# Kernel tuning notes

Hardware: AMD Instinct MI355X
Metric: run time of the kernel (lower is better)

## Reference

```python
import jax, jax.numpy as jnp
import numpy as np
import math

H = 16          # num_heads
BS = 512        # block_size


def setup_inputs() -> dict:
    key = jax.random.key(0)
    ks = jax.random.split(key, 5)
    B, S, D = 2, 8192, 1024
    return {
        "x": jax.random.normal(ks[0], (B, S, D), dtype=jnp.float32),
        "W_qkv": jax.random.normal(ks[1], (D, 3 * D), dtype=jnp.float32) * (1.0 / math.sqrt(D)),
        "b_qkv": jax.random.normal(ks[2], (3 * D,), dtype=jnp.float32) * 0.02,
        "W_out": jax.random.normal(ks[3], (D, D), dtype=jnp.float32) * (1.0 / math.sqrt(D)),
        "b_out": jax.random.normal(ks[4], (D,), dtype=jnp.float32) * 0.02,
    }


def reference(x, W_qkv, b_qkv, W_out, b_out):
    B, S, D = x.shape
    hd = D // H
    nb = S // BS  # S chosen divisible by block_size, so no padding branch
    scale = 1.0 / math.sqrt(hd)

    qkv = (x @ W_qkv + b_qkv).reshape(B, S, 3, H, hd)
    qkv = jnp.transpose(qkv, (2, 0, 3, 1, 4))  # [3, B, H, S, hd]
    q, k, v = qkv[0], qkv[1], qkv[2]

    # split into blocks: [B, H, nb, BS, hd]
    qb = q.reshape(B, H, nb, BS, hd)
    kb = k.reshape(B, H, nb, BS, hd)
    vb = v.reshape(B, H, nb, BS, hd)

    # local block attention (separate softmax, as in original)
    s1 = jnp.einsum('bhnid,bhnjd->bhnij', qb, kb) * scale
    o1 = jnp.einsum('bhnij,bhnjd->bhnid', jax.nn.softmax(s1, axis=-1), vb)

    # next-block (ring) attention with its own softmax, then summed
    kn = jnp.roll(kb, -1, axis=2)
    vn = jnp.roll(vb, -1, axis=2)
    s2 = jnp.einsum('bhnid,bhnjd->bhnij', qb, kn) * scale
    o2 = jnp.einsum('bhnij,bhnjd->bhnid', jax.nn.softmax(s2, axis=-1), vn)

    out = (o1 + o2).reshape(B, H, S, hd)            # [B, H, S, hd]
    out = jnp.transpose(out, (0, 2, 1, 3)).reshape(B, S, D)
    return out @ W_out + b_out
```

## Files before the change

kernel.cpp:

```cpp
#include <hip/hip_runtime.h>
#include <hip/hip_bf16.h>

typedef __attribute__((ext_vector_type(4))) float f32x4;
typedef __attribute__((ext_vector_type(8))) short s16x8;
typedef __attribute__((address_space(3))) unsigned int lds_uint;
typedef __attribute__((address_space(1))) const unsigned int g_uint;

static __device__ __forceinline__ unsigned short f2b(float f) {
    union { __hip_bfloat16 h; unsigned short u; } c;
    c.h = __float2bfloat16(f);
    return c.u;
}

static __device__ __forceinline__ void async_copy16(const void* gsrc, void* ldst) {
    __builtin_amdgcn_global_load_lds((g_uint*)gsrc, (lds_uint*)ldst, 16, 0, 0);
}

__global__ __launch_bounds__(256) void cvt_x_kernel(const float* __restrict__ x,
                                                    unsigned short* __restrict__ xb) {
    long i = ((long)blockIdx.x * 256 + threadIdx.x) * 8;
    float4 a = *(const float4*)(x + i);
    float4 b = *(const float4*)(x + i + 4);
    union { unsigned short s[8]; s16x8 v; } o;
    o.s[0] = f2b(a.x); o.s[1] = f2b(a.y); o.s[2] = f2b(a.z); o.s[3] = f2b(a.w);
    o.s[4] = f2b(b.x); o.s[5] = f2b(b.y); o.s[6] = f2b(b.z); o.s[7] = f2b(b.w);
    *(s16x8*)(xb + i) = o.v;
}

__global__ __launch_bounds__(256) void cvt_wT_kernel(const float* __restrict__ W,
                                                     unsigned short* __restrict__ Wt,
                                                     int K, int N) {
    __shared__ float T[64][65];
    int nbk = K >> 6;
    int bk = blockIdx.x % nbk;
    int bn = blockIdx.x / nbk;
    int t = threadIdx.x;
    int r = t >> 4, c4 = (t & 15) << 2;
#pragma unroll
    for (int rd = 0; rd < 4; ++rd) {
        int row = rd * 16 + r;
        float4 v = *(const float4*)(W + (long)(bk * 64 + row) * N + bn * 64 + c4);
        T[row][c4 + 0] = v.x; T[row][c4 + 1] = v.y;
        T[row][c4 + 2] = v.z; T[row][c4 + 3] = v.w;
    }
    __syncthreads();
#pragma unroll
    for (int rd = 0; rd < 4; ++rd) {
        int nrow = rd * 16 + r;
        union { unsigned short s[4]; unsigned long long u; } o;
#pragma unroll
        for (int j = 0; j < 4; ++j) o.s[j] = f2b(T[c4 + j][nrow]);
        *(unsigned long long*)(Wt + (long)(bn * 64 + nrow) * K + bk * 64 + c4) = o.u;
    }
}

__global__ __launch_bounds__(256) void gemm_qkv_kernel(const unsigned short* __restrict__ A,
                                                       const unsigned short* __restrict__ Bt,
                                                       const float* __restrict__ bias,
                                                       unsigned short* __restrict__ qkb,
                                                       unsigned short* __restrict__ vT) {
    const int K = 1024;
    __shared__ unsigned short As[128 * 32];
    __shared__ unsigned short Bs[128 * 32];
    const int tid = threadIdx.x;
    const int w = tid >> 6, l = tid & 63;
    const int c = l & 15, g = l >> 4;
    const int tm = blockIdx.x / 24, tn = blockIdx.x % 24;
    const long m0 = (long)tm << 7, n0 = (long)tn << 7;

    f32x4 acc[4][4];
#pragma unroll
    for (int i = 0; i < 4; ++i)
#pragma unroll
        for (int j = 0; j < 4; ++j) acc[i][j] = (f32x4){0.f, 0.f, 0.f, 0.f};

    const int arow = tid >> 2, ac8 = (tid & 3) << 3;
    for (int k0 = 0; k0 < K; k0 += 32) {
        __syncthreads();
#pragma unroll
        for (int rd = 0; rd < 2; ++rd) {
            int row = arow + rd * 64;
            int off = (rd * 256 + tid) * 16;
            async_copy16(A + (m0 + row) * (long)K + k0 + ac8, (char*)As + off);
            async_copy16(Bt + (n0 + row) * (long)K + k0 + ac8, (char*)Bs + off);
        }
        __syncthreads();
        s16x8 af[4], bf_[4];
#pragma unroll
        for (int i = 0; i < 4; ++i) {
            af[i]  = *(const s16x8*)((const char*)As + ((w >> 1) * 64 + i * 16 + c) * 64 + g * 16);
            bf_[i] = *(const s16x8*)((const char*)Bs + ((w & 1) * 64 + i * 16 + c) * 64 + g * 16);
        }
#pragma unroll
        for (int i = 0; i < 4; ++i)
#pragma unroll
            for (int j = 0; j < 4; ++j)
                acc[i][j] = __builtin_amdgcn_mfma_f32_16x16x32_bf16(af[i], bf_[j], acc[i][j], 0, 0, 0);
    }

    if (n0 < 2048) {
#pragma unroll
        for (int j = 0; j < 4; ++j) {
            int n = (int)n0 + (w & 1) * 64 + j * 16 + c;
            float bv = bias[n];
#pragma unroll
            for (int i = 0; i < 4; ++i)
#pragma unroll
                for (int r = 0; r < 4; ++r) {
                    long m = m0 + (w >> 1) * 64 + i * 16 + 4 * g + r;
                    qkb[m * 2048 + n] = f2b(acc[i][j][r] + bv);
                }
        }
    } else {
#pragma unroll
        for (int j = 0; j < 4; ++j) {
            int n = (int)n0 + (w & 1) * 64 + j * 16 + c;
            float bv = bias[n];
            int h = (n - 2048) >> 6, hd = n & 63;
#pragma unroll
            for (int i = 0; i < 4; ++i) {
                long m = m0 + (w >> 1) * 64 + i * 16 + 4 * g;
                long bb = m >> 13;
                long s = m & 8191;
                union { unsigned short sh[4]; unsigned long long u; } o;
#pragma unroll
                for (int r = 0; r < 4; ++r) o.sh[r] = f2b(acc[i][j][r] + bv);
                *(unsigned long long*)(vT + ((bb * 16 + h) * 64 + hd) * 8192 + s) = o.u;
            }
        }
    }
}

__global__ __launch_bounds__(256) void gemm_out_kernel(const unsigned short* __restrict__ A,
                                                       const unsigned short* __restrict__ Bt,
                                                       const float* __restrict__ bias,
                                                       float* __restrict__ C,
                                                       int M, int N, int K) {
    __shared__ unsigned short As[128 * 32];
    __shared__ unsigned short Bs[128 * 32];
    const int tid = threadIdx.x;
    const int w = tid >> 6, l = tid & 63;
    const int c = l & 15, g = l >> 4;
    const int ntile = N >> 7;
    const int tm = blockIdx.x / ntile, tn = blockIdx.x % ntile;
    const long m0 = (long)tm << 7, n0 = (long)tn << 7;

    f32x4 acc[4][4];
#pragma unroll
    for (int i = 0; i < 4; ++i)
#pragma unroll
        for (int j = 0; j < 4; ++j) acc[i][j] = (f32x4){0.f, 0.f, 0.f, 0.f};

    const int arow = tid >> 2, ac8 = (tid & 3) << 3;
    for (int k0 = 0; k0 < K; k0 += 32) {
        __syncthreads();
#pragma unroll
        for (int rd = 0; rd < 2; ++rd) {
            int row = arow + rd * 64;
            int off = (rd * 256 + tid) * 16;
            async_copy16(A + (m0 + row) * (long)K + k0 + ac8, (char*)As + off);
            async_copy16(Bt + (n0 + row) * (long)K + k0 + ac8, (char*)Bs + off);
        }
        __syncthreads();
        s16x8 af[4], bf_[4];
#pragma unroll
        for (int i = 0; i < 4; ++i) {
            af[i]  = *(const s16x8*)((const char*)As + ((w >> 1) * 64 + i * 16 + c) * 64 + g * 16);
            bf_[i] = *(const s16x8*)((const char*)Bs + ((w & 1) * 64 + i * 16 + c) * 64 + g * 16);
        }
#pragma unroll
        for (int i = 0; i < 4; ++i)
#pragma unroll
            for (int j = 0; j < 4; ++j)
                acc[i][j] = __builtin_amdgcn_mfma_f32_16x16x32_bf16(af[i], bf_[j], acc[i][j], 0, 0, 0);
    }
#pragma unroll
    for (int j = 0; j < 4; ++j) {
        int n = (int)n0 + (w & 1) * 64 + j * 16 + c;
        float bv = bias[n];
#pragma unroll
        for (int i = 0; i < 4; ++i)
#pragma unroll
            for (int r = 0; r < 4; ++r) {
                long m = m0 + (w >> 1) * 64 + i * 16 + 4 * g + r;
                C[m * (long)N + n] = acc[i][j][r] + bv;
            }
    }
}

__global__ __launch_bounds__(256) void attn_kernel(const unsigned short* __restrict__ qkb,
                                                   const unsigned short* __restrict__ vT,
                                                   unsigned short* __restrict__ outp) {
    __shared__ unsigned short Ks[64 * 72];
    __shared__ unsigned short VTs[64 * 72];
    __shared__ unsigned short Pws[4][16 * 72];
    const int bid = blockIdx.x;
    const int qt = bid & 7;
    const int nblk = (bid >> 3) & 15;
    const int h = (bid >> 7) & 15;
    const int b = bid >> 11;
    const int tid = threadIdx.x;
    const int w = tid >> 6, l = tid & 63;
    const int c = l & 15, g = l >> 4;

    const long qrow = (long)b * 8192 + nblk * 512 + qt * 64 + w * 16 + c;
    const unsigned short* qp = qkb + qrow * 2048 + h * 64;
    const s16x8 qf0 = *(const s16x8*)(qp + g * 8);
    const s16x8 qf1 = *(const s16x8*)(qp + 32 + g * 8);

    char* pw = (char*)(&Pws[w][0]);
    const float C2 = 0.125f * 1.44269504088896f;

    float outv[16];
#pragma unroll
    for (int i = 0; i < 16; ++i) outv[i] = 0.f;

    const int cc = tid & 7;
    const int rbase = tid >> 3;

    for (int p = 0; p < 2; ++p) {
        const int kblk = (nblk + p) & 15;
        const unsigned short* Kg = qkb + ((long)b * 8192 + kblk * 512) * 2048 + 1024 + h * 64;
        const unsigned short* Vg = vT + ((long)(b * 16 + h) * 64) * 8192 + kblk * 512;

        f32x4 oac[4];
#pragma unroll
        for (int i = 0; i < 4; ++i) oac[i] = (f32x4){0.f, 0.f, 0.f, 0.f};
        float mrun = -1e30f, lrun = 0.f;

        for (int ch = 0; ch < 8; ++ch) {
            s16x8 kreg[2], vreg[2];
#pragma unroll
            for (int rd = 0; rd < 2; ++rd) {
                int row = rd * 32 + rbase;
                kreg[rd] = *(const s16x8*)(Kg + (long)(ch * 64 + row) * 2048 + cc * 8);
                vreg[rd] = *(const s16x8*)(Vg + (long)row * 8192 + ch * 64 + cc * 8);
            }
            __syncthreads();
#pragma unroll
            for (int rd = 0; rd < 2; ++rd) {
                int row = rd * 32 + rbase;
                *(s16x8*)((char*)Ks + row * 144 + cc * 16) = kreg[rd];
                *(s16x8*)((char*)VTs + row * 144 + cc * 16) = vreg[rd];
            }
            __syncthreads();

            f32x4 sac[4];
#pragma unroll
            for (int i = 0; i < 4; ++i) sac[i] = (f32x4){0.f, 0.f, 0.f, 0.f};
#pragma unroll
            for (int kt = 0; kt < 4; ++kt) {
                const char* kr = (const char*)Ks + (kt * 16 + c) * 144;
                s16x8 a0 = *(const s16x8*)(kr + g * 16);
                s16x8 a1 = *(const s16x8*)(kr + 64 + g * 16);
                sac[kt] = __builtin_amdgcn_mfma_f32_16x16x32_bf16(a0, qf0, sac[kt], 0, 0, 0);
                sac[kt] = __builtin_amdgcn_mfma_f32_16x16x32_bf16(a1, qf1, sac[kt], 0, 0, 0);
            }

            float mx = sac[0][0];
#pragma unroll
            for (int kt = 0; kt < 4; ++kt)
#pragma unroll
                for (int r = 0; r < 4; ++r) mx = fmaxf(mx, sac[kt][r]);
            mx = fmaxf(mx, __shfl_xor(mx, 16, 64));
            mx = fmaxf(mx, __shfl_xor(mx, 32, 64));
            float mnew = fmaxf(mrun, mx);
            float alpha = exp2f((mrun - mnew) * C2);

            float ls = 0.f;
#pragma unroll
            for (int kt = 0; kt < 4; ++kt) {
                union { unsigned short sh[4]; unsigned long long u; } pk;
#pragma unroll
                for (int r = 0; r < 4; ++r) {
                    float e = exp2f((sac[kt][r] - mnew) * C2);
                    ls += e;
                    pk.sh[r] = f2b(e);
                }
                *(unsigned long long*)(pw + c * 144 + kt * 32 + g * 8) = pk.u;
            }
            ls += __shfl_xor(ls, 16, 64);
            ls += __shfl_xor(ls, 32, 64);
            lrun = lrun * alpha + ls;
            mrun = mnew;
#pragma unroll
            for (int i = 0; i < 4; ++i) oac[i] *= alpha;

#pragma unroll
            for (int kf = 0; kf < 2; ++kf) {
                s16x8 pf = *(const s16x8*)(pw + c * 144 + kf * 64 + g * 16);
#pragma unroll
                for (int ht = 0; ht < 4; ++ht) {
                    s16x8 vf = *(const s16x8*)((const char*)VTs + (ht * 16 + c) * 144 + kf * 64 + g * 16);
                    oac[ht] = __builtin_amdgcn_mfma_f32_16x16x32_bf16(vf, pf, oac[ht], 0, 0, 0);
                }
            }
        }

        float inv = 1.f / lrun;
#pragma unroll
        for (int i = 0; i < 16; ++i) outv[i] += oac[i >> 2][i & 3] * inv;
    }

    unsigned short* op = outp + qrow * 1024 + h * 64;
#pragma unroll
    for (int ht = 0; ht < 4; ++ht) {
        union { unsigned short sh[4]; unsigned long long u; } o;
#pragma unroll
        for (int r = 0; r < 4; ++r) o.sh[r] = f2b(outv[ht * 4 + r]);
        *(unsigned long long*)(op + ht * 16 + 4 * g) = o.u;
    }
}

extern "C" void kernel_launch(void* const* d_in, const int* in_sizes, int n_in,
                              void* d_out, int out_size, void* d_ws, size_t ws_size,
                              hipStream_t stream) {
    const float* x    = (const float*)d_in[0];
    const float* Wqkv = (const float*)d_in[1];
    const float* bqkv = (const float*)d_in[2];
    const float* Wout = (const float*)d_in[3];
    const float* bout = (const float*)d_in[4];
    float* out = (float*)d_out;

    char* ws = (char*)d_ws;
    unsigned short* xbf   = (unsigned short*)ws;
    unsigned short* wqkvT = (unsigned short*)(ws + 33554432);
    unsigned short* woutT = (unsigned short*)(ws + 39845888);
    unsigned short* qkb   = (unsigned short*)(ws + 41943040);
    unsigned short* vT    = (unsigned short*)(ws + 109051904);
    unsigned short* attn  = xbf;

    cvt_x_kernel<<<8192, 256, 0, stream>>>(x, xbf);
    cvt_wT_kernel<<<(1024 / 64) * (3072 / 64), 256, 0, stream>>>(Wqkv, wqkvT, 1024, 3072);
    cvt_wT_kernel<<<(1024 / 64) * (1024 / 64), 256, 0, stream>>>(Wout, woutT, 1024, 1024);
    gemm_qkv_kernel<<<128 * 24, 256, 0, stream>>>(xbf, wqkvT, bqkv, qkb, vT);
    attn_kernel<<<4096, 256, 0, stream>>>(qkb, vT, attn);
    gemm_out_kernel<<<128 * 8, 256, 0, stream>>>(attn, woutT, bout, out, 16384, 1024, 1024);
}
```

Baseline: 501.1 us.

## Double query rows per attention wave, prefetch K/V, and remap workgroups per XCD

The attention kernel now handles 32 query rows per wave (128 per workgroup), so each K/V chunk staged in LDS is reused by twice as many MFMAs, and the grid is halved. The two key blocks are merged into one 16-iteration loop that register-prefetches the next K/V chunk while the current one is computed, with the softmax state reset at the block boundary. Both GEMMs and the attention kernel remap blockIdx so that consecutive tiles land on the same XCD, aiming for better L2 locality. This raises register pressure and halves the number of workgroups, which may reduce occupancy.

```diff
diff --git a/kernel.cpp b/kernel.cpp
--- a/kernel.cpp
+++ b/kernel.cpp
@@ -65,7 +65,8 @@
     const int tid = threadIdx.x;
     const int w = tid >> 6, l = tid & 63;
     const int c = l & 15, g = l >> 4;
-    const int tm = blockIdx.x / 24, tn = blockIdx.x % 24;
+    const int wgid = (blockIdx.x & 7) * 384 + (blockIdx.x >> 3);
+    const int tm = wgid / 24, tn = wgid % 24;
     const long m0 = (long)tm << 7, n0 = (long)tn << 7;
 
     f32x4 acc[4][4];
@@ -142,7 +143,9 @@
     const int w = tid >> 6, l = tid & 63;
     const int c = l & 15, g = l >> 4;
     const int ntile = N >> 7;
-    const int tm = blockIdx.x / ntile, tn = blockIdx.x % ntile;
+    const int cpx = gridDim.x >> 3;
+    const int wgid = (blockIdx.x & 7) * cpx + (blockIdx.x >> 3);
+    const int tm = wgid / ntile, tn = wgid % ntile;
     const long m0 = (long)tm << 7, n0 = (long)tn << 7;
 
     f32x4 acc[4][4];
@@ -193,122 +196,160 @@
                                                    unsigned short* __restrict__ outp) {
     __shared__ unsigned short Ks[64 * 72];
     __shared__ unsigned short VTs[64 * 72];
-    __shared__ unsigned short Pws[4][16 * 72];
+    __shared__ unsigned short Pws[4][32 * 72];
     const int bid = blockIdx.x;
-    const int qt = bid & 7;
-    const int nblk = (bid >> 3) & 15;
-    const int h = (bid >> 7) & 15;
-    const int b = bid >> 11;
+    const int wgid = (bid & 7) * 256 + (bid >> 3);
+    const int qt = wgid & 3;
+    const int nblk = (wgid >> 2) & 15;
+    const int h = (wgid >> 6) & 15;
+    const int b = wgid >> 10;
     const int tid = threadIdx.x;
     const int w = tid >> 6, l = tid & 63;
     const int c = l & 15, g = l >> 4;
 
-    const long qrow = (long)b * 8192 + nblk * 512 + qt * 64 + w * 16 + c;
-    const unsigned short* qp = qkb + qrow * 2048 + h * 64;
-    const s16x8 qf0 = *(const s16x8*)(qp + g * 8);
-    const s16x8 qf1 = *(const s16x8*)(qp + 32 + g * 8);
+    const long qrow0 = (long)b * 8192 + nblk * 512 + qt * 128 + w * 32 + c;
+    s16x8 qf[2][2];
+#pragma unroll
+    for (int qg = 0; qg < 2; ++qg) {
+        const unsigned short* qp = qkb + (qrow0 + qg * 16) * 2048 + h * 64;
+        qf[qg][0] = *(const s16x8*)(qp + g * 8);
+        qf[qg][1] = *(const s16x8*)(qp + 32 + g * 8);
+    }
 
     char* pw = (char*)(&Pws[w][0]);
     const float C2 = 0.125f * 1.44269504088896f;
 
-    float outv[16];
-#pragma unroll
-    for (int i = 0; i < 16; ++i) outv[i] = 0.f;
-
     const int cc = tid & 7;
     const int rbase = tid >> 3;
-
-    for (int p = 0; p < 2; ++p) {
-        const int kblk = (nblk + p) & 15;
-        const unsigned short* Kg = qkb + ((long)b * 8192 + kblk * 512) * 2048 + 1024 + h * 64;
-        const unsigned short* Vg = vT + ((long)(b * 16 + h) * 64) * 8192 + kblk * 512;
-
-        f32x4 oac[4];
-#pragma unroll
-        for (int i = 0; i < 4; ++i) oac[i] = (f32x4){0.f, 0.f, 0.f, 0.f};
-        float mrun = -1e30f, lrun = 0.f;
-
-        for (int ch = 0; ch < 8; ++ch) {
-            s16x8 kreg[2], vreg[2];
-#pragma unroll
-            for (int rd = 0; rd < 2; ++rd) {
-                int row = rd * 32 + rbase;
-                kreg[rd] = *(const s16x8*)(Kg + (long)(ch * 64 + row) * 2048 + cc * 8);
-                vreg[rd] = *(const s16x8*)(Vg + (long)row * 8192 + ch * 64 + cc * 8);
-            }
-            __syncthreads();
-#pragma unroll
-            for (int rd = 0; rd < 2; ++rd) {
-                int row = rd * 32 + rbase;
-                *(s16x8*)((char*)Ks + row * 144 + cc * 16) = kreg[rd];
-                *(s16x8*)((char*)VTs + row * 144 + cc * 16) = vreg[rd];
-            }
-            __syncthreads();
-
-            f32x4 sac[4];
-#pragma unroll
-            for (int i = 0; i < 4; ++i) sac[i] = (f32x4){0.f, 0.f, 0.f, 0.f};
-#pragma unroll
-            for (int kt = 0; kt < 4; ++kt) {
-                const char* kr = (const char*)Ks + (kt * 16 + c) * 144;
-                s16x8 a0 = *(const s16x8*)(kr + g * 16);
-                s16x8 a1 = *(const s16x8*)(kr + 64 + g * 16);
-                sac[kt] = __builtin_amdgcn_mfma_f32_16x16x32_bf16(a0, qf0, sac[kt], 0, 0, 0);
-                sac[kt] = __builtin_amdgcn_mfma_f32_16x16x32_bf16(a1, qf1, sac[kt], 0, 0, 0);
-            }
-
-            float mx = sac[0][0];
+    char* kwp = (char*)Ks + rbase * 144 + cc * 16;
+    char* vwp = (char*)VTs + rbase * 144 + cc * 16;
+
+    const int kb1 = (nblk + 1) & 15;
+    const unsigned short* Kg0 = qkb + ((long)b * 8192 + nblk * 512) * 2048 + 1024 + h * 64
+                                + (long)rbase * 2048 + cc * 8;
+    const unsigned short* Kg1 = qkb + ((long)b * 8192 + kb1 * 512) * 2048 + 1024 + h * 64
+                                + (long)rbase * 2048 + cc * 8;
+    const unsigned short* Vg0 = vT + ((long)(b * 16 + h) * 64 + rbase) * 8192 + nblk * 512 + cc * 8;
+    const unsigned short* Vg1 = vT + ((long)(b * 16 + h) * 64 + rbase) * 8192 + kb1 * 512 + cc * 8;
+
+    float outv[2][16];
+#pragma unroll
+    for (int qg = 0; qg < 2; ++qg)
+#pragma unroll
+        for (int i = 0; i < 16; ++i) outv[qg][i] = 0.f;
+
+    f32x4 oac[2][4];
+#pragma unroll
+    for (int qg = 0; qg < 2; ++qg)
+#pragma unroll
+        for (int i = 0; i < 4; ++i) oac[qg][i] = (f32x4){0.f, 0.f, 0.f, 0.f};
+    float mrun[2] = {-3e38f, -3e38f}, lrun[2] = {0.f, 0.f};
+
+    s16x8 kreg0 = *(const s16x8*)(Kg0);
+    s16x8 kreg1 = *(const s16x8*)(Kg0 + 32 * 2048);
+    s16x8 vreg0 = *(const s16x8*)(Vg0);
+    s16x8 vreg1 = *(const s16x8*)(Vg0 + 32 * 8192);
+
+    for (int it = 0; it < 16; ++it) {
+        __syncthreads();
+        *(s16x8*)(kwp) = kreg0;
+        *(s16x8*)(kwp + 32 * 144) = kreg1;
+        *(s16x8*)(vwp) = vreg0;
+        *(s16x8*)(vwp + 32 * 144) = vreg1;
+        {
+            int itn = it + 1;
+            const unsigned short* kn = ((itn & 8) ? Kg1 : Kg0) + ((itn & 7) << 17);
+            const unsigned short* vn = ((itn & 8) ? Vg1 : Vg0) + ((itn & 7) << 6);
+            kreg0 = *(const s16x8*)(kn);
+            kreg1 = *(const s16x8*)(kn + 32 * 2048);
+            vreg0 = *(const s16x8*)(vn);
+            vreg1 = *(const s16x8*)(vn + 32 * 8192);
+        }
+        __syncthreads();
+
+        f32x4 sac[2][4];
+#pragma unroll
+        for (int qg = 0; qg < 2; ++qg)
+#pragma unroll
+            for (int i = 0; i < 4; ++i) sac[qg][i] = (f32x4){0.f, 0.f, 0.f, 0.f};
+#pragma unroll
+        for (int kt = 0; kt < 4; ++kt) {
+            const char* kr = (const char*)Ks + (kt * 16 + c) * 144 + g * 16;
+            s16x8 a0 = *(const s16x8*)(kr);
+            s16x8 a1 = *(const s16x8*)(kr + 64);
+            sac[0][kt] = __builtin_amdgcn_mfma_f32_16x16x32_bf16(a0, qf[0][0], sac[0][kt], 0, 0, 0);
+            sac[0][kt] = __builtin_amdgcn_mfma_f32_16x16x32_bf16(a1, qf[0][1], sac[0][kt], 0, 0, 0);
+            sac[1][kt] = __builtin_amdgcn_mfma_f32_16x16x32_bf16(a0, qf[1][0], sac[1][kt], 0, 0, 0);
+            sac[1][kt] = __builtin_amdgcn_mfma_f32_16x16x32_bf16(a1, qf[1][1], sac[1][kt], 0, 0, 0);
+        }
+
+#pragma unroll
+        for (int qg = 0; qg < 2; ++qg) {
+            float mx = sac[qg][0][0];
 #pragma unroll
             for (int kt = 0; kt < 4; ++kt)
 #pragma unroll
-                for (int r = 0; r < 4; ++r) mx = fmaxf(mx, sac[kt][r]);
+                for (int r = 0; r < 4; ++r) mx = fmaxf(mx, sac[qg][kt][r]);
             mx = fmaxf(mx, __shfl_xor(mx, 16, 64));
             mx = fmaxf(mx, __shfl_xor(mx, 32, 64));
-            float mnew = fmaxf(mrun, mx);
-            float alpha = exp2f((mrun - mnew) * C2);
-
+            float mnew = fmaxf(mrun[qg], mx);
+            float alpha = exp2f((mrun[qg] - mnew) * C2);
             float ls = 0.f;
 #pragma unroll
             for (int kt = 0; kt < 4; ++kt) {
                 union { unsigned short sh[4]; unsigned long long u; } pk;
 #pragma unroll
                 for (int r = 0; r < 4; ++r) {
-                    float e = exp2f((sac[kt][r] - mnew) * C2);
+                    float e = exp2f((sac[qg][kt][r] - mnew) * C2);
                     ls += e;
                     pk.sh[r] = f2b(e);
                 }
-                *(unsigned long long*)(pw + c * 144 + kt * 32 + g * 8) = pk.u;
+                *(unsigned long long*)(pw + (qg * 16 + c) * 144 + kt * 32 + g * 8) = pk.u;
             }
             ls += __shfl_xor(ls, 16, 64);
             ls += __shfl_xor(ls, 32, 64);
-            lrun = lrun * alpha + ls;
-            mrun = mnew;
-#pragma unroll
-            for (int i = 0; i < 4; ++i) oac[i] *= alpha;
-
-#pragma unroll
-            for (int kf = 0; kf < 2; ++kf) {
-                s16x8 pf = *(const s16x8*)(pw + c * 144 + kf * 64 + g * 16);
-#pragma unroll
-                for (int ht = 0; ht < 4; ++ht) {
-                    s16x8 vf = *(const s16x8*)((const char*)VTs + (ht * 16 + c) * 144 + kf * 64 + g * 16);
-                    oac[ht] = __builtin_amdgcn_mfma_f32_16x16x32_bf16(vf, pf, oac[ht], 0, 0, 0);
-                }
-            }
-        }
-
-        float inv = 1.f / lrun;
-#pragma unroll
-        for (int i = 0; i < 16; ++i) outv[i] += oac[i >> 2][i & 3] * inv;
-    }
-
-    unsigned short* op = outp + qrow * 1024 + h * 64;
-#pragma unroll
-    for (int ht = 0; ht < 4; ++ht) {
-        union { unsigned short sh[4]; unsigned long long u; } o;
-#pragma unroll
-        for (int r = 0; r < 4; ++r) o.sh[r] = f2b(outv[ht * 4 + r]);
-        *(unsigned long long*)(op + ht * 16 + 4 * g) = o.u;
+            lrun[qg] = lrun[qg] * alpha + ls;
+            mrun[qg] = mnew;
+#pragma unroll
+            for (int i = 0; i < 4; ++i) oac[qg][i] *= alpha;
+        }
+
+#pragma unroll
+        for (int kf = 0; kf < 2; ++kf) {
+            s16x8 pf0 = *(const s16x8*)(pw + c * 144 + kf * 64 + g * 16);
+            s16x8 pf1 = *(const s16x8*)(pw + (16 + c) * 144 + kf * 64 + g * 16);
+#pragma unroll
+            for (int ht = 0; ht < 4; ++ht) {
+                s16x8 vf = *(const s16x8*)((const char*)VTs + (ht * 16 + c) * 144 + kf * 64 + g * 16);
+                oac[0][ht] = __builtin_amdgcn_mfma_f32_16x16x32_bf16(vf, pf0, oac[0][ht], 0, 0, 0);
+                oac[1][ht] = __builtin_amdgcn_mfma_f32_16x16x32_bf16(vf, pf1, oac[1][ht], 0, 0, 0);
+            }
+        }
+
+        if ((it & 7) == 7) {
+#pragma unroll
+            for (int qg = 0; qg < 2; ++qg) {
+                float inv = 1.f / lrun[qg];
+#pragma unroll
+                for (int i = 0; i < 16; ++i) outv[qg][i] += oac[qg][i >> 2][i & 3] * inv;
+#pragma unroll
+                for (int i = 0; i < 4; ++i) oac[qg][i] = (f32x4){0.f, 0.f, 0.f, 0.f};
+                mrun[qg] = -3e38f;
+                lrun[qg] = 0.f;
+            }
+        }
+    }
+
+#pragma unroll
+    for (int qg = 0; qg < 2; ++qg) {
+        unsigned short* op = outp + (qrow0 + qg * 16) * 1024 + h * 64;
+#pragma unroll
+        for (int ht = 0; ht < 4; ++ht) {
+            union { unsigned short sh[4]; unsigned long long u; } o;
+#pragma unroll
+            for (int r = 0; r < 4; ++r) o.sh[r] = f2b(outv[qg][ht * 4 + r]);
+            *(unsigned long long*)(op + ht * 16 + 4 * g) = o.u;
+        }
     }
 }
 
@@ -334,6 +375,6 @@
     cvt_wT_kernel<<<(1024 / 64) * (3072 / 64), 256, 0, stream>>>(Wqkv, wqkvT, 1024, 3072);
     cvt_wT_kernel<<<(1024 / 64) * (1024 / 64), 256, 0, stream>>>(Wout, woutT, 1024, 1024);
     gemm_qkv_kernel<<<128 * 24, 256, 0, stream>>>(xbf, wqkvT, bqkv, qkb, vT);
-    attn_kernel<<<4096, 256, 0, stream>>>(qkb, vT, attn);
+    attn_kernel<<<2048, 256, 0, stream>>>(qkb, vT, attn);
     gemm_out_kernel<<<128 * 8, 256, 0, stream>>>(attn, woutT, bout, out, 16384, 1024, 1024);
 }
```

New measurement: 487.5 us. -2.7%, faster.
